# Performance work log

Hardware: AMD Instinct MI355X
Metric: run time of the kernel (lower is better)

Reference implementation:

```python
import jax, jax.numpy as jnp
import numpy as np

DECAY = 0.99
EPS = 1e-05


def setup_inputs() -> dict:
    key = jax.random.key(0)
    k1, k2 = jax.random.split(key)
    B, C, H, W = 16, 64, 32, 32
    K = 8192
    z_e = jax.random.normal(k1, (B, C, H, W), dtype=jnp.float32)
    embedding = jax.random.normal(k2, (K, C), dtype=jnp.float32)
    cluster_size = jnp.zeros((K,), dtype=jnp.float32)
    embedding_avg = embedding  # initialized as a clone of the codebook
    return {"z_e": z_e, "embedding": embedding, "cluster_size": cluster_size,
            "embedding_avg": embedding_avg}


def reference(z_e, embedding, cluster_size, embedding_avg):
    B, C, H, W = z_e.shape
    K = embedding.shape[0]
    # [N, C] tokens
    z_flat = jnp.transpose(z_e, (0, 2, 3, 1)).reshape(-1, C)
    d = ((z_flat * z_flat).sum(-1, keepdims=True)
         - 2.0 * (z_flat @ embedding.T)
         + (embedding * embedding).sum(-1))
    indices = jnp.argmin(d, axis=1)  # [N] int
    z_q_flat = embedding[indices]    # [N, C]
    z_q = jnp.transpose(z_q_flat.reshape(B, H, W, C), (0, 3, 1, 2))
    # EMA codebook update (training path); one-hot matmuls expressed as segment sums
    counts = jax.ops.segment_sum(jnp.ones(z_flat.shape[0], dtype=z_flat.dtype),
                                 indices, num_segments=K)            # encodings.sum(0)
    dw = jax.ops.segment_sum(z_flat, indices, num_segments=K)        # encodings.T @ z_flat
    new_cluster_size = DECAY * cluster_size + (1.0 - DECAY) * counts
    new_embedding_avg = DECAY * embedding_avg + (1.0 - DECAY) * dw
    n = new_cluster_size.sum()
    cs = (new_cluster_size + EPS) / (n + K * EPS) * n
    new_embedding = new_embedding_avg / cs[:, None]
    # straight-through estimator
    z_q_st = z_e + jax.lax.stop_gradient(z_q - z_e)
    return (z_q_st, indices.reshape(B, H * W), z_q,
            new_embedding, new_cluster_size, new_embedding_avg)
```

## Files before the change

### kernel.cpp

```cpp
#include <hip/hip_runtime.h>

#define DECAYF 0.99f
#define OMDF   0.01f
#define TAU    3.5e-2f

typedef unsigned int u32;
typedef unsigned long long u64;
typedef __attribute__((ext_vector_type(8))) _Float16 f16x8;
typedef __attribute__((ext_vector_type(4))) float f32x4;

#define EN_OFF     0
#define EFRAG_OFF  32768
#define IDX_OFF    32768
#define CNT8K_OFF  1081344
#define OFFS_OFF   1114112
#define FILLP_OFF  1146880
#define TOKL_OFF   1179648
#define BEST1_OFF  2129920
#define BEST2_OFF  3178496
#define NSUM_OFF   3702784

__device__ __forceinline__ u64 enc_pair(float s, int idx) {
  u32 u = __float_as_uint(s);
  u = (u & 0x80000000u) ? ~u : (u | 0x80000000u);
  return ((u64)u << 32) | (u32)(~idx);
}
__device__ __forceinline__ float dec_score(u64 e) {
  u32 u = (u32)(e >> 32);
  u = (u & 0x80000000u) ? (u & 0x7fffffffu) : ~u;
  return __uint_as_float(u);
}
__device__ __forceinline__ int dec_idx(u64 e) { return (int)(~(u32)e); }
__device__ __forceinline__ unsigned short f2h(float f) {
  union { _Float16 h; unsigned short u; } v;
  v.h = (_Float16)f;
  return v.u;
}
__device__ __forceinline__ float exact_dot(const float* __restrict__ sx,
                                           const float* __restrict__ emb, int k) {
  const float4* e = (const float4*)(emb + (size_t)k * 64);
  float a = 0.f;
#pragma unroll
  for (int q = 0; q < 16; ++q) {
    float4 v = e[q];
    a = fmaf(sx[4 * q],     v.x, a);
    a = fmaf(sx[4 * q + 1], v.y, a);
    a = fmaf(sx[4 * q + 2], v.z, a);
    a = fmaf(sx[4 * q + 3], v.w, a);
  }
  return a;
}

__global__ __launch_bounds__(256) void k_prep(const float* __restrict__ emb,
                                              const float* __restrict__ cs_in,
                                              const float* __restrict__ avg_in,
                                              const float* __restrict__ z_e,
                                              float* __restrict__ en,
                                              unsigned char* __restrict__ efrag,
                                              unsigned char* __restrict__ zfrag,
                                              float* __restrict__ out4,
                                              float* __restrict__ out5,
                                              float* __restrict__ nsum,
                                              int* __restrict__ cnt8k) {
  __shared__ float warr[4];
  __shared__ float sx[64][129];
  int bid = blockIdx.x;
  int t = threadIdx.x;
  if (bid < 512) {
    int tid = bid * 256 + t;
    int k = tid >> 4, q = tid & 15;
    float4 v = ((const float4*)emb)[tid];
    ushort4 hv;
    hv.x = f2h(v.x); hv.y = f2h(v.y); hv.z = f2h(v.z); hv.w = f2h(v.w);
    size_t off = (size_t)(k >> 4) * 2048 + (size_t)(q >> 3) * 1024
               + (size_t)((q >> 1) & 3) * 256 + (size_t)(k & 15) * 16
               + (size_t)(q & 1) * 8;
    *(ushort4*)(efrag + off) = hv;
    float s = v.x * v.x + v.y * v.y + v.z * v.z + v.w * v.w;
    s += __shfl_xor(s, 1, 16);
    s += __shfl_xor(s, 2, 16);
    s += __shfl_xor(s, 4, 16);
    s += __shfl_xor(s, 8, 16);
    if (q == 0) en[k] = 0.5f * s;
  } else if (bid < 1031) {
    int tid = (bid - 512) * 256 + t;
    if (tid < 131072) {
      float4 v = ((const float4*)avg_in)[tid];
      v.x *= DECAYF; v.y *= DECAYF; v.z *= DECAYF; v.w *= DECAYF;
      ((float4*)out5)[tid] = v;
    }
  } else if (bid == 1031) {
    float s = 0.f;
#pragma unroll
    for (int q = 0; q < 8; ++q) {
      int idx = q * 256 + t;
      float4 v = ((const float4*)cs_in)[idx];
      v.x *= DECAYF; v.y *= DECAYF; v.z *= DECAYF; v.w *= DECAYF;
      ((float4*)out4)[idx] = v;
      s += v.x + v.y + v.z + v.w;
      ((int4*)cnt8k)[idx] = make_int4(0, 0, 0, 0);
    }
    s += __shfl_xor(s, 1, 64);
    s += __shfl_xor(s, 2, 64);
    s += __shfl_xor(s, 4, 64);
    s += __shfl_xor(s, 8, 64);
    s += __shfl_xor(s, 16, 64);
    s += __shfl_xor(s, 32, 64);
    if ((t & 63) == 0) warr[t >> 6] = s;
    __syncthreads();
    if (t == 0) *nsum = warr[0] + warr[1] + warr[2] + warr[3];
  } else {
    int n0 = (bid - 1032) * 128;
    int b = n0 >> 10, hwb = n0 & 1023;
#pragma unroll
    for (int r = 0; r < 8; ++r) {
      int g = r * 256 + t;
      int c = g >> 5, f4 = g & 31;
      float4 v = *(const float4*)(z_e + ((size_t)b << 16) + ((size_t)c << 10)
                                  + hwb + f4 * 4);
      sx[c][f4 * 4 + 0] = v.x;
      sx[c][f4 * 4 + 1] = v.y;
      sx[c][f4 * 4 + 2] = v.z;
      sx[c][f4 * 4 + 3] = v.w;
    }
    __syncthreads();
#pragma unroll
    for (int r = 0; r < 4; ++r) {
      int id = r * 256 + t;
      int nl = id & 127, k = id >> 7;
      int n = n0 + nl;
      unsigned short u[8];
#pragma unroll
      for (int j = 0; j < 8; ++j) u[j] = f2h(sx[k * 8 + j][nl]);
      size_t off = (size_t)(n >> 4) * 2048 + (size_t)(k >> 2) * 1024
                 + (size_t)(k & 3) * 256 + (size_t)(n & 15) * 16;
      *(ushort4*)(zfrag + off)     = make_ushort4(u[0], u[1], u[2], u[3]);
      *(ushort4*)(zfrag + off + 8) = make_ushort4(u[4], u[5], u[6], u[7]);
    }
  }
}

__global__ __launch_bounds__(256) void k_argmin_mfma(
    const unsigned char* __restrict__ zfrag,
    const unsigned char* __restrict__ efrag,
    const float* __restrict__ en, u64* __restrict__ best1,
    float* __restrict__ best2) {
  alignas(16) __shared__ unsigned char sbuf[2][8192];
  __shared__ float sen[1024];
  const int tb = blockIdx.x >> 3;
  const int sl = blockIdx.x & 7;
  const int wave = threadIdx.x >> 6, lane = threadIdx.x & 63;
  const int col = lane & 15, g4 = lane >> 4;
  const int token0 = tb * 64 + wave * 16;
  const int scb = sl << 10;

  ((float4*)sen)[threadIdx.x] = ((const float4*)(en + scb))[threadIdx.x];

  f16x8 a0, a1;
  {
    const unsigned char* zb = zfrag + ((size_t)(tb * 4 + wave)) * 2048
                            + (size_t)g4 * 256 + (size_t)col * 16;
    a0 = *(const f16x8*)(zb);
    a1 = *(const f16x8*)(zb + 1024);
  }
  float b1[4], b2[4];
#pragma unroll
  for (int r = 0; r < 4; ++r) { b1[r] = -3.0e38f; b2[r] = -3.0e38f; }

  const unsigned char* gbase0 = efrag + (size_t)scb * 128;
  auto stage = [&](int ib, int buf) {
    const unsigned char* g = gbase0 + (size_t)ib * 8192 + (size_t)wave * 2048;
#pragma unroll
    for (int it = 0; it < 2; ++it) {
      __builtin_amdgcn_global_load_lds(
          (const __attribute__((address_space(1))) u32*)(g + it * 1024 + lane * 16),
          (__attribute__((address_space(3))) u32*)(&sbuf[buf][wave * 2048 + it * 1024]),
          16, 0, 0);
    }
  };
  stage(0, 0);
  for (int ib = 0; ib < 16; ++ib) {
    __syncthreads();
    if (ib < 15) stage(ib + 1, (ib + 1) & 1);
    const unsigned char* sb0 = &sbuf[ib & 1][0];
#pragma unroll
    for (int ct = 0; ct < 4; ++ct) {
      const int t = ib * 4 + ct;
      const float negen = -sen[t * 16 + col];
      f16x8 bf0 = *(const f16x8*)(sb0 + ct * 2048 + lane * 16);
      f16x8 bf1 = *(const f16x8*)(sb0 + ct * 2048 + 1024 + lane * 16);
      f32x4 acc;
#pragma unroll
      for (int r = 0; r < 4; ++r) acc[r] = negen;
      acc = __builtin_amdgcn_mfma_f32_16x16x32_f16(a0, bf0, acc, 0, 0, 0);
      acc = __builtin_amdgcn_mfma_f32_16x16x32_f16(a1, bf1, acc, 0, 0, 0);
      const u32 emb6 = (u32)(63 - t);
#pragma unroll
      for (int r = 0; r < 4; ++r) {
        float f0 = __uint_as_float((__float_as_uint(acc[r]) & 0xFFFFFFC0u) | emb6);
        b2[r] = __builtin_amdgcn_fmed3f(f0, b1[r], b2[r]);
        b1[r] = fmaxf(b1[r], f0);
      }
    }
  }
  int mi[4];
#pragma unroll
  for (int r = 0; r < 4; ++r) mi[r] = col;
#pragma unroll
  for (int st = 1; st < 16; st <<= 1) {
#pragma unroll
    for (int r = 0; r < 4; ++r) {
      float ob1 = __shfl_xor(b1[r], st, 64);
      float ob2 = __shfl_xor(b2[r], st, 64);
      int omi = __shfl_xor(mi[r], st, 64);
      bool ogt = ob1 > b1[r];
      b2[r] = fmaxf(fminf(b1[r], ob1), fmaxf(b2[r], ob2));
      mi[r] = ogt ? omi : mi[r];
      b1[r] = fmaxf(b1[r], ob1);
    }
  }
  if (col == 0) {
#pragma unroll
    for (int r = 0; r < 4; ++r) {
      int token = token0 + g4 * 4 + r;
      int t = 63 - (int)(__float_as_uint(b1[r]) & 63u);
      int gcode = scb + t * 16 + mi[r];
      best1[(size_t)sl * 16384 + token] = enc_pair(b1[r], gcode);
      best2[(size_t)sl * 16384 + token] = b2[r];
    }
  }
}

__global__ __launch_bounds__(256) void k_resfix(const float* __restrict__ z_e,
                                                const float* __restrict__ emb,
                                                const float* __restrict__ en,
                                                const u64* __restrict__ best1,
                                                const float* __restrict__ best2,
                                                int* __restrict__ idxa,
                                                int* __restrict__ cnt8k) {
  __shared__ float sxr[64];
  __shared__ int sidx[64];
  __shared__ int flist[64];
  __shared__ float fth[64];
  __shared__ int nflag;
  __shared__ u32 fmask;
  __shared__ u64 red;
  int t = threadIdx.x;
  int n0 = blockIdx.x * 64;
  if (t == 0) nflag = 0;
  __syncthreads();
  if (t < 64) {
    int n = n0 + t;
    u64 e[8];
#pragma unroll
    for (int s = 0; s < 8; ++s) e[s] = best1[(size_t)s * 16384 + n];
    u64 top = e[0];
#pragma unroll
    for (int s = 1; s < 8; ++s) top = e[s] > top ? e[s] : top;
    float second = -3.0e38f;
#pragma unroll
    for (int s = 0; s < 8; ++s)
      second = fmaxf(second, best2[(size_t)s * 16384 + n]);
#pragma unroll
    for (int s = 0; s < 8; ++s)
      if (e[s] != top) second = fmaxf(second, dec_score(e[s]));
    idxa[n] = dec_idx(top);
    sidx[t] = dec_idx(top);
    if (dec_score(top) - second < TAU) {
      int p = atomicAdd(&nflag, 1);
      flist[p] = n;
      fth[p] = dec_score(top);
    }
  }
  __syncthreads();
  int nf = nflag;
  for (int i = 0; i < nf; ++i) {
    int n = flist[i];
    float theta = fth[i] - TAU;
    if (t == 0) { fmask = 0; red = 0ull; }
    if (t < 64) {
      sxr[t] = z_e[((size_t)(n >> 10) << 16) + ((size_t)t << 10) + (n & 1023)];
    }
    __syncthreads();
    u64 myb = 0ull;
    if (t < 8) {
      u64 es = best1[(size_t)t * 16384 + n];
      if (best2[(size_t)t * 16384 + n] >= theta) atomicOr(&fmask, 1u << t);
      if (dec_score(es) >= theta) {
        int k = dec_idx(es);
        float a = exact_dot(sxr, emb, k) - en[k];
        myb = enc_pair(a, k);
      }
    }
    __syncthreads();
    u32 fm = fmask;
    while (fm) {
      int s = __ffs(fm) - 1;
      fm &= fm - 1;
      int k0 = (s << 10) + t;
      float a0 = exact_dot(sxr, emb, k0)       - en[k0];
      float a1 = exact_dot(sxr, emb, k0 + 256) - en[k0 + 256];
      float a2 = exact_dot(sxr, emb, k0 + 512) - en[k0 + 512];
      float a3 = exact_dot(sxr, emb, k0 + 768) - en[k0 + 768];
      u64 m0 = enc_pair(a0, k0),       m1 = enc_pair(a1, k0 + 256);
      u64 m2 = enc_pair(a2, k0 + 512), m3 = enc_pair(a3, k0 + 768);
      u64 ma = m0 > m1 ? m0 : m1, mb = m2 > m3 ? m2 : m3;
      u64 mm = ma > mb ? ma : mb;
      myb = mm > myb ? mm : myb;
    }
    if (myb) atomicMax(&red, myb);
    __syncthreads();
    if (t == 0) {
      idxa[n] = dec_idx(red);
      sidx[n - n0] = dec_idx(red);
    }
    __syncthreads();
  }
  if (t < 64) atomicAdd(&cnt8k[sidx[t]], 1);
}

__global__ __launch_bounds__(256) void k_scan(const int* __restrict__ cnt8k,
                                              int* __restrict__ offs,
                                              int* __restrict__ fillp) {
  __shared__ int part[256];
  int t = threadIdx.x;
  int loc[32];
  int s = 0;
#pragma unroll
  for (int i = 0; i < 32; ++i) {
    loc[i] = s;
    s += cnt8k[t * 32 + i];
  }
  part[t] = s;
  __syncthreads();
  for (int st = 1; st < 256; st <<= 1) {
    int add = (t >= st) ? part[t - st] : 0;
    __syncthreads();
    part[t] += add;
    __syncthreads();
  }
  int base = part[t] - s;
#pragma unroll
  for (int i = 0; i < 32; ++i) {
    int o = base + loc[i];
    offs[t * 32 + i]  = o;
    fillp[t * 32 + i] = o;
  }
}

__global__ __launch_bounds__(256) void k_fill(const int* __restrict__ idxa,
                                              int* __restrict__ fillp,
                                              int* __restrict__ tokl) {
  int n = blockIdx.x * 256 + threadIdx.x;
  int idx = idxa[n];
  int pos = atomicAdd(&fillp[idx], 1);
  tokl[pos] = n;
}

__global__ __launch_bounds__(256) void k_gather(const float* __restrict__ z_e,
                                                const float* __restrict__ emb,
                                                const int* __restrict__ idxa,
                                                const int* __restrict__ cnt8k,
                                                const int* __restrict__ offs,
                                                const int* __restrict__ tokl,
                                                float* __restrict__ out0,
                                                float* __restrict__ out1,
                                                float* __restrict__ out2,
                                                float* __restrict__ out5) {
  int tid = blockIdx.x * 256 + threadIdx.x;
  {
    int hw4 = tid & 255;
    int c   = (tid >> 8) & 63;
    int b   = tid >> 14;
    int n0  = (b << 10) + (hw4 << 2);
    size_t off = ((size_t)b << 16) + ((size_t)c << 10) + ((size_t)hw4 << 2);
    float4 z = *(const float4*)(z_e + off);
    int i0 = idxa[n0], i1 = idxa[n0 + 1], i2 = idxa[n0 + 2], i3 = idxa[n0 + 3];
    float4 q;
    q.x = emb[(size_t)i0 * 64 + c];
    q.y = emb[(size_t)i1 * 64 + c];
    q.z = emb[(size_t)i2 * 64 + c];
    q.w = emb[(size_t)i3 * 64 + c];
    float4 st;
    st.x = z.x + (q.x - z.x);
    st.y = z.y + (q.y - z.y);
    st.z = z.z + (q.z - z.z);
    st.w = z.w + (q.w - z.w);
    *(float4*)(out2 + off) = q;
    *(float4*)(out0 + off) = st;
    if (c == 0) {
      float4 f = make_float4((float)i0, (float)i1, (float)i2, (float)i3);
      *(float4*)(out1 + n0) = f;
    }
  }
  {
    int wv = blockIdx.x * 4 + (threadIdx.x >> 6);
    int lane = threadIdx.x & 63;
#pragma unroll
    for (int rep = 0; rep < 2; ++rep) {
      int k = wv * 2 + rep;
      int cnt = cnt8k[k];
      int o = offs[k];
      float sum = 0.f;
      for (int j = 0; j < cnt; ++j) {
        int n = tokl[o + j];
        sum += z_e[((size_t)(n >> 10) << 16) + ((size_t)lane << 10) + (n & 1023)];
      }
      if (cnt > 0) {
        size_t oi = (size_t)k * 64 + lane;
        out5[oi] = fmaf(OMDF, sum, out5[oi]);
      }
    }
  }
}

__global__ __launch_bounds__(256) void k_final(float* __restrict__ out4,
                                               const float* __restrict__ out5,
                                               const float* __restrict__ nsum,
                                               const int* __restrict__ cnt8k,
                                               float* __restrict__ out3) {
  int tid = blockIdx.x * 256 + threadIdx.x;
  int k = tid >> 4;
  float ncsf = fmaf(OMDF, (float)cnt8k[k], out4[k]);
  double nn  = (double)*nsum + 163.84;
  double cs  = ((double)ncsf + 1e-5) / (nn + 8192.0 * 1e-5) * nn;
  float inv  = (float)(1.0 / cs);
  float4 v = ((const float4*)out5)[tid];
  v.x *= inv; v.y *= inv; v.z *= inv; v.w *= inv;
  ((float4*)out3)[tid] = v;
  if ((tid & 15) == 0) out4[k] = ncsf;
}

extern "C" void kernel_launch(void* const* d_in, const int* in_sizes, int n_in,
                              void* d_out, int out_size, void* d_ws, size_t ws_size,
                              hipStream_t stream) {
  const float* z_e    = (const float*)d_in[0];
  const float* emb    = (const float*)d_in[1];
  const float* cs_in  = (const float*)d_in[2];
  const float* avg_in = (const float*)d_in[3];

  float* out  = (float*)d_out;
  float* out0 = out;
  float* out1 = out0 + 1048576;
  float* out2 = out1 + 16384;
  float* out3 = out2 + 1048576;
  float* out4 = out3 + 524288;
  float* out5 = out4 + 8192;

  char* ws = (char*)d_ws;
  float* en            = (float*)(ws + EN_OFF);
  unsigned char* efrag = (unsigned char*)(ws + EFRAG_OFF);
  int* idxa            = (int*)(ws + IDX_OFF);
  int* cnt8k           = (int*)(ws + CNT8K_OFF);
  int* offs            = (int*)(ws + OFFS_OFF);
  int* fillp           = (int*)(ws + FILLP_OFF);
  int* tokl            = (int*)(ws + TOKL_OFF);
  u64* best1           = (u64*)(ws + BEST1_OFF);
  float* best2         = (float*)(ws + BEST2_OFF);
  float* nsum          = (float*)(ws + NSUM_OFF);
  unsigned char* zfrag = (unsigned char*)out0;

  k_prep       <<<1160, 256, 0, stream>>>(emb, cs_in, avg_in, z_e, en, efrag,
                                          zfrag, out4, out5, nsum, cnt8k);
  k_argmin_mfma<<<2048, 256, 0, stream>>>(zfrag, efrag, en, best1, best2);
  k_resfix     <<<256,  256, 0, stream>>>(z_e, emb, en, best1, best2, idxa, cnt8k);
  k_scan       <<<1,    256, 0, stream>>>(cnt8k, offs, fillp);
  k_fill       <<<64,   256, 0, stream>>>(idxa, fillp, tokl);
  k_gather     <<<1024, 256, 0, stream>>>(z_e, emb, idxa, cnt8k, offs, tokl,
                                          out0, out1, out2, out5);
  k_final      <<<512,  256, 0, stream>>>(out4, out5, nsum, cnt8k, out3);
}
```

Baseline: 180.8 us.

## Replace count/scan/fill token lists with direct float atomics for EMA scatter

Drops the per-code histogram, the single-block prefix scan and the token-list fill kernels. Each gathered token now atomically adds 0.01*z into the embedding average and 0.01 into the cluster size, and the final kernel reads those sums directly. The z_e transpose blocks in the prep kernel are also halved to 64 tokens per block. This removes two launches and a serial scan, but adds contention on float atomics for popular codes and makes the summation order nondeterministic.

```diff
diff --git a/kernel.cpp b/kernel.cpp
--- a/kernel.cpp
+++ b/kernel.cpp
@@ -12,10 +12,6 @@
 #define EN_OFF     0
 #define EFRAG_OFF  32768
 #define IDX_OFF    32768
-#define CNT8K_OFF  1081344
-#define OFFS_OFF   1114112
-#define FILLP_OFF  1146880
-#define TOKL_OFF   1179648
 #define BEST1_OFF  2129920
 #define BEST2_OFF  3178496
 #define NSUM_OFF   3702784
@@ -60,10 +56,9 @@
                                               unsigned char* __restrict__ zfrag,
                                               float* __restrict__ out4,
                                               float* __restrict__ out5,
-                                              float* __restrict__ nsum,
-                                              int* __restrict__ cnt8k) {
+                                              float* __restrict__ nsum) {
   __shared__ float warr[4];
-  __shared__ float sx[64][129];
+  __shared__ float sx[64][65];
   int bid = blockIdx.x;
   int t = threadIdx.x;
   if (bid < 512) {
@@ -98,7 +93,6 @@
       v.x *= DECAYF; v.y *= DECAYF; v.z *= DECAYF; v.w *= DECAYF;
       ((float4*)out4)[idx] = v;
       s += v.x + v.y + v.z + v.w;
-      ((int4*)cnt8k)[idx] = make_int4(0, 0, 0, 0);
     }
     s += __shfl_xor(s, 1, 64);
     s += __shfl_xor(s, 2, 64);
@@ -110,12 +104,12 @@
     __syncthreads();
     if (t == 0) *nsum = warr[0] + warr[1] + warr[2] + warr[3];
   } else {
-    int n0 = (bid - 1032) * 128;
+    int n0 = (bid - 1032) * 64;
     int b = n0 >> 10, hwb = n0 & 1023;
 #pragma unroll
-    for (int r = 0; r < 8; ++r) {
+    for (int r = 0; r < 4; ++r) {
       int g = r * 256 + t;
-      int c = g >> 5, f4 = g & 31;
+      int c = g >> 4, f4 = g & 15;
       float4 v = *(const float4*)(z_e + ((size_t)b << 16) + ((size_t)c << 10)
                                   + hwb + f4 * 4);
       sx[c][f4 * 4 + 0] = v.x;
@@ -125,9 +119,9 @@
     }
     __syncthreads();
 #pragma unroll
-    for (int r = 0; r < 4; ++r) {
+    for (int r = 0; r < 2; ++r) {
       int id = r * 256 + t;
-      int nl = id & 127, k = id >> 7;
+      int nl = id & 63, k = id >> 6;
       int n = n0 + nl;
       unsigned short u[8];
 #pragma unroll
@@ -236,10 +230,8 @@
                                                 const float* __restrict__ en,
                                                 const u64* __restrict__ best1,
                                                 const float* __restrict__ best2,
-                                                int* __restrict__ idxa,
-                                                int* __restrict__ cnt8k) {
+                                                int* __restrict__ idxa) {
   __shared__ float sxr[64];
-  __shared__ int sidx[64];
   __shared__ int flist[64];
   __shared__ float fth[64];
   __shared__ int nflag;
@@ -265,7 +257,6 @@
     for (int s = 0; s < 8; ++s)
       if (e[s] != top) second = fmaxf(second, dec_score(e[s]));
     idxa[n] = dec_idx(top);
-    sidx[t] = dec_idx(top);
     if (dec_score(top) - second < TAU) {
       int p = atomicAdd(&nflag, 1);
       flist[p] = n;
@@ -310,62 +301,18 @@
     }
     if (myb) atomicMax(&red, myb);
     __syncthreads();
-    if (t == 0) {
-      idxa[n] = dec_idx(red);
-      sidx[n - n0] = dec_idx(red);
-    }
-    __syncthreads();
-  }
-  if (t < 64) atomicAdd(&cnt8k[sidx[t]], 1);
-}
-
-__global__ __launch_bounds__(256) void k_scan(const int* __restrict__ cnt8k,
-                                              int* __restrict__ offs,
-                                              int* __restrict__ fillp) {
-  __shared__ int part[256];
-  int t = threadIdx.x;
-  int loc[32];
-  int s = 0;
-#pragma unroll
-  for (int i = 0; i < 32; ++i) {
-    loc[i] = s;
-    s += cnt8k[t * 32 + i];
-  }
-  part[t] = s;
-  __syncthreads();
-  for (int st = 1; st < 256; st <<= 1) {
-    int add = (t >= st) ? part[t - st] : 0;
-    __syncthreads();
-    part[t] += add;
-    __syncthreads();
-  }
-  int base = part[t] - s;
-#pragma unroll
-  for (int i = 0; i < 32; ++i) {
-    int o = base + loc[i];
-    offs[t * 32 + i]  = o;
-    fillp[t * 32 + i] = o;
-  }
-}
-
-__global__ __launch_bounds__(256) void k_fill(const int* __restrict__ idxa,
-                                              int* __restrict__ fillp,
-                                              int* __restrict__ tokl) {
-  int n = blockIdx.x * 256 + threadIdx.x;
-  int idx = idxa[n];
-  int pos = atomicAdd(&fillp[idx], 1);
-  tokl[pos] = n;
+    if (t == 0) idxa[n] = dec_idx(red);
+    __syncthreads();
+  }
 }
 
 __global__ __launch_bounds__(256) void k_gather(const float* __restrict__ z_e,
                                                 const float* __restrict__ emb,
                                                 const int* __restrict__ idxa,
-                                                const int* __restrict__ cnt8k,
-                                                const int* __restrict__ offs,
-                                                const int* __restrict__ tokl,
                                                 float* __restrict__ out0,
                                                 float* __restrict__ out1,
                                                 float* __restrict__ out2,
+                                                float* __restrict__ out4,
                                                 float* __restrict__ out5) {
   int tid = blockIdx.x * 256 + threadIdx.x;
   {
@@ -394,41 +341,33 @@
     }
   }
   {
-    int wv = blockIdx.x * 4 + (threadIdx.x >> 6);
-    int lane = threadIdx.x & 63;
-#pragma unroll
-    for (int rep = 0; rep < 2; ++rep) {
-      int k = wv * 2 + rep;
-      int cnt = cnt8k[k];
-      int o = offs[k];
-      float sum = 0.f;
-      for (int j = 0; j < cnt; ++j) {
-        int n = tokl[o + j];
-        sum += z_e[((size_t)(n >> 10) << 16) + ((size_t)lane << 10) + (n & 1023)];
-      }
-      if (cnt > 0) {
-        size_t oi = (size_t)k * 64 + lane;
-        out5[oi] = fmaf(OMDF, sum, out5[oi]);
-      }
-    }
-  }
-}
-
-__global__ __launch_bounds__(256) void k_final(float* __restrict__ out4,
+    int c = tid & 63;
+    int nb = (tid >> 6) * 4;
+#pragma unroll
+    for (int i = 0; i < 4; ++i) {
+      int n = nb + i;
+      int idx = idxa[n];
+      int b = n >> 10, hw = n & 1023;
+      float x = z_e[((size_t)b << 16) + ((size_t)c << 10) + hw];
+      atomicAdd(out5 + (size_t)idx * 64 + c, OMDF * x);
+      if (c == 0) atomicAdd(out4 + idx, OMDF);
+    }
+  }
+}
+
+__global__ __launch_bounds__(256) void k_final(const float* __restrict__ out4,
                                                const float* __restrict__ out5,
                                                const float* __restrict__ nsum,
-                                               const int* __restrict__ cnt8k,
                                                float* __restrict__ out3) {
   int tid = blockIdx.x * 256 + threadIdx.x;
   int k = tid >> 4;
-  float ncsf = fmaf(OMDF, (float)cnt8k[k], out4[k]);
   double nn  = (double)*nsum + 163.84;
-  double cs  = ((double)ncsf + 1e-5) / (nn + 8192.0 * 1e-5) * nn;
+  double ncs = (double)out4[k];
+  double cs  = (ncs + 1e-5) / (nn + 8192.0 * 1e-5) * nn;
   float inv  = (float)(1.0 / cs);
   float4 v = ((const float4*)out5)[tid];
   v.x *= inv; v.y *= inv; v.z *= inv; v.w *= inv;
   ((float4*)out3)[tid] = v;
-  if ((tid & 15) == 0) out4[k] = ncsf;
 }
 
 extern "C" void kernel_launch(void* const* d_in, const int* in_sizes, int n_in,
@@ -451,22 +390,16 @@
   float* en            = (float*)(ws + EN_OFF);
   unsigned char* efrag = (unsigned char*)(ws + EFRAG_OFF);
   int* idxa            = (int*)(ws + IDX_OFF);
-  int* cnt8k           = (int*)(ws + CNT8K_OFF);
-  int* offs            = (int*)(ws + OFFS_OFF);
-  int* fillp           = (int*)(ws + FILLP_OFF);
-  int* tokl            = (int*)(ws + TOKL_OFF);
   u64* best1           = (u64*)(ws + BEST1_OFF);
   float* best2         = (float*)(ws + BEST2_OFF);
   float* nsum          = (float*)(ws + NSUM_OFF);
   unsigned char* zfrag = (unsigned char*)out0;
 
-  k_prep       <<<1160, 256, 0, stream>>>(emb, cs_in, avg_in, z_e, en, efrag,
-                                          zfrag, out4, out5, nsum, cnt8k);
+  k_prep       <<<1288, 256, 0, stream>>>(emb, cs_in, avg_in, z_e, en, efrag,
+                                          zfrag, out4, out5, nsum);
   k_argmin_mfma<<<2048, 256, 0, stream>>>(zfrag, efrag, en, best1, best2);
-  k_resfix     <<<256,  256, 0, stream>>>(z_e, emb, en, best1, best2, idxa, cnt8k);
-  k_scan       <<<1,    256, 0, stream>>>(cnt8k, offs, fillp);
-  k_fill       <<<64,   256, 0, stream>>>(idxa, fillp, tokl);
-  k_gather     <<<1024, 256, 0, stream>>>(z_e, emb, idxa, cnt8k, offs, tokl,
-                                          out0, out1, out2, out5);
-  k_final      <<<512,  256, 0, stream>>>(out4, out5, nsum, cnt8k, out3);
-}
+  k_resfix     <<<256,  256, 0, stream>>>(z_e, emb, en, best1, best2, idxa);
+  k_gather     <<<1024, 256, 0, stream>>>(z_e, emb, idxa, out0, out1, out2,
+                                          out4, out5);
+  k_final      <<<512,  256, 0, stream>>>(out4, out5, nsum, out3);
+}
```

Result: faster. 154.7 us (-14.5%).
